# Kernel optimization log

Measured on AMD Instinct MI355X. Metric: run time of the kernel, lower is better.

Reference implementation:

```python
import jax, jax.numpy as jnp
import numpy as np

B, T, N, F, E, L = 2, 2, 10000, 128, 160000, 2


def setup_inputs() -> dict:
    key = jax.random.key(0)
    k = jax.random.split(key, 6)
    feature = jax.random.normal(k[0], (B, T, N, F), jnp.float32)
    edge_src = jax.random.randint(k[1], (E,), 0, N, jnp.int32)
    edge_dst = jax.random.randint(k[2], (E,), 0, N, jnp.int32)
    s = 1.0 / np.sqrt(F).astype(np.float32)
    W_self = jax.random.normal(k[3], (L, F, F), jnp.float32) * s
    W_neigh = jax.random.normal(k[4], (L, F, F), jnp.float32) * s
    b = jnp.zeros((L, F), jnp.float32)
    return dict(feature=feature, W_self=W_self, W_neigh=W_neigh, b=b,
                edge_src=edge_src, edge_dst=edge_dst)


def reference(feature, W_self, W_neigh, b, edge_src, edge_dst):
    # feature: [B, T, N, Fin]; edge (src -> dst) as in dgl.from_scipy(csr).
    Bs, Ts, Ns, Fin = feature.shape
    num_layers = W_self.shape[0]
    # in-degree per dst node; mean over zero in-degree nodes is 0 (DGL semantics)
    deg = jax.ops.segment_sum(jnp.ones(edge_dst.shape, jnp.float32), edge_dst,
                              num_segments=Ns)
    inv_deg = jnp.where(deg > 0, 1.0 / jnp.maximum(deg, 1.0), 0.0)  # [N]
    # node-major layout for gather/scatter: [N, B, T, F]
    h = jnp.transpose(feature, (2, 0, 1, 3))
    for l in range(num_layers):
        msg = h[edge_src]  # [E, B, T, F] irregular gather
        agg = jax.ops.segment_sum(msg, edge_dst, num_segments=Ns)
        h_neigh = agg * inv_deg[:, None, None, None]  # mean aggregation
        h = (jnp.einsum('nbtf,fg->nbtg', h, W_self[l])
             + jnp.einsum('nbtf,fg->nbtg', h_neigh, W_neigh[l])
             + b[l])
    # res.permute(0,2,1,3) in torch -> [B, T, N, Fout]
    return jnp.transpose(h, (1, 2, 0, 3))
```

## Files before the change

kernel.cpp:

```cpp
#include <hip/hip_runtime.h>

constexpr int N_  = 10000;
constexpr int F_  = 128;
constexpr int E_  = 160000;
constexpr int BT_ = 4;
constexpr int M_  = N_ * BT_;
constexpr int CAP = 64;

typedef __attribute__((ext_vector_type(8))) short bf16x8;
typedef __attribute__((ext_vector_type(4))) float f32x4;
typedef __attribute__((ext_vector_type(2))) float f32x2;
typedef __attribute__((ext_vector_type(8))) unsigned short u16x8;

static __device__ inline unsigned short f2bf(float f) {
    union { float f; unsigned int i; } v; v.f = f;
    unsigned int x = v.i;
    return (unsigned short)((x + 0x7fffu + ((x >> 16) & 1u)) >> 16);
}


__global__ __launch_bounds__(256) void k_pre(const float4* __restrict__ feat,
        unsigned short* __restrict__ h0, unsigned char* __restrict__ h8,
        unsigned char* __restrict__ h18z,
        const int* __restrict__ src, const int* __restrict__ dst,
        int* __restrict__ cursor, int* __restrict__ bucket,
        const float* __restrict__ Wself, const float* __restrict__ Wneigh,
        unsigned short* __restrict__ Wp) {
    const int b = blockIdx.x;
    const int tid = threadIdx.x;
    if (b < 625) {
        int e = b * 256 + tid;
        int d = dst[e];
        int p = atomicAdd(&cursor[d], 1);
        if (p < CAP) bucket[d * CAP + p] = src[e];
    } else if (b < 657) {
        if (b == 625) {
            if (tid < 64) {
                uint2 z; z.x = 0u; z.y = 0u;
                *(uint2*)(h8 + (size_t)N_ * 512 + tid * 8) = z;
            } else if (tid < 128) {
                uint2 z; z.x = 0u; z.y = 0u;
                *(uint2*)(h18z + (size_t)N_ * 512 + (tid - 64) * 8) = z;
            }
        }
        int t = (b - 625) * 256 + tid;
        int mat = t >> 11;
        int r = t & 2047;
        int kb = r >> 9;
        int nb = (r >> 6) & 7;
        int lane = r & 63;
        int l = mat >> 1, s = mat & 1;
        const float* W = (s ? Wneigh : Wself) + (size_t)l * F_ * F_;
        int k0 = kb * 32 + (lane >> 4) * 8;
        int n  = nb * 16 + (lane & 15);
        unsigned short* dstp = Wp + (size_t)mat * 16384 +
                               (size_t)((kb * 8 + nb) * 64 + lane) * 8;
#pragma unroll
        for (int j = 0; j < 8; j++) dstp[j] = f2bf(W[(size_t)(k0 + j) * F_ + n]);
    } else {
        int i = (b - 657) * 256 + tid;
        int f4 = i & 31;
        int m  = i >> 5;
        int n  = m >> 2;
        int bt = m & 3;
        float4 v = feat[(bt * N_ + n) * 32 + f4];
        ushort4 o;
        o.x = f2bf(v.x); o.y = f2bf(v.y); o.z = f2bf(v.z); o.w = f2bf(v.w);
        *(ushort4*)(h0 + (size_t)m * 128 + f4 * 4) = o;
        int w0 = __builtin_amdgcn_cvt_pk_fp8_f32(v.x, v.y, 0, false);
        int w1 = __builtin_amdgcn_cvt_pk_fp8_f32(v.z, v.w, w0, true);
        *(unsigned int*)(h8 + (size_t)m * 128 + f4 * 4) = (unsigned int)w1;
    }
}


template <bool LAST>
__global__ __launch_bounds__(256) void k_fused(const unsigned short* __restrict__ h,
        const unsigned char* __restrict__ g8, unsigned char* __restrict__ s8out,
        const int* __restrict__ cursor, const int* __restrict__ bucket,
        const unsigned short* __restrict__ Wp, const float* __restrict__ bias,
        void* __restrict__ outv) {
    __shared__ unsigned short aggs[4][4][136];
    const int tid  = threadIdx.x;
    const int wave = tid >> 6, lane = tid & 63;
    const int m0   = blockIdx.x * 16;
    const int node0 = m0 >> 2;
    const int col  = lane & 15;
    const int quad = lane >> 4;

    const unsigned short* A0 = h + (size_t)(m0 + col) * 128 + quad * 8;
    bf16x8 aA[4];
#pragma unroll
    for (int kb = 0; kb < 4; kb++) aA[kb] = *(const bf16x8*)(A0 + kb * 32);

    const int n   = node0 + wave;
    const int deg = cursor[n];
    const int nn  = deg < CAP ? deg : CAP;
    const int nn8 = (nn + 7) & ~7;
    int idx = bucket[n * CAP + (lane < nn ? lane : 0)];

    float acc8[8] = {0.f, 0.f, 0.f, 0.f, 0.f, 0.f, 0.f, 0.f};
    for (int e0 = 0; e0 < nn8; e0 += 8) {
#pragma unroll
        for (int u = 0; u < 8; u++) {
            int e = e0 + u;
            int s = (e < nn) ? __builtin_amdgcn_readlane(idx, e) : N_;
            uint2 a8 = *(const uint2*)(g8 + (size_t)s * 512 + lane * 8);
            f32x2 p0 = __builtin_amdgcn_cvt_pk_f32_fp8(a8.x, false);
            f32x2 p1 = __builtin_amdgcn_cvt_pk_f32_fp8(a8.x, true);
            f32x2 p2 = __builtin_amdgcn_cvt_pk_f32_fp8(a8.y, false);
            f32x2 p3 = __builtin_amdgcn_cvt_pk_f32_fp8(a8.y, true);
            acc8[0] += p0.x; acc8[1] += p0.y;
            acc8[2] += p1.x; acc8[3] += p1.y;
            acc8[4] += p2.x; acc8[5] += p2.y;
            acc8[6] += p3.x; acc8[7] += p3.y;
        }
    }
    {
        float w = (deg > 0) ? 1.0f / (float)deg : 0.0f;
        u16x8 o;
#pragma unroll
        for (int j = 0; j < 8; j++) o[j] = f2bf(acc8[j] * w);
        *(u16x8*)&aggs[wave][lane >> 4][(lane & 15) * 8] = o;
    }
    __syncthreads();

    const int np = wave;
    f32x4 acc[2];
#pragma unroll
    for (int j = 0; j < 2; j++) {
        float b = bias[(np * 2 + j) * 16 + col];
        acc[j] = (f32x4){b, b, b, b};
    }

    const unsigned short* As = &aggs[col >> 2][col & 3][quad * 8];
    const unsigned short* B0 = Wp + (size_t)lane * 8;
    const unsigned short* B1 = B0 + 16384;

#pragma unroll
    for (int kb = 0; kb < 4; kb++) {
        bf16x8 a = aA[kb];
#pragma unroll
        for (int j = 0; j < 2; j++) {
            int nb = np * 2 + j;
            bf16x8 b = *(const bf16x8*)(B0 + (size_t)((kb * 8 + nb) * 64) * 8);
            acc[j] = __builtin_amdgcn_mfma_f32_16x16x32_bf16(a, b, acc[j], 0, 0, 0);
        }
    }
#pragma unroll
    for (int kb = 0; kb < 4; kb++) {
        bf16x8 a = *(const bf16x8*)(As + kb * 32);
#pragma unroll
        for (int j = 0; j < 2; j++) {
            int nb = np * 2 + j;
            bf16x8 b = *(const bf16x8*)(B1 + (size_t)((kb * 8 + nb) * 64) * 8);
            acc[j] = __builtin_amdgcn_mfma_f32_16x16x32_bf16(a, b, acc[j], 0, 0, 0);
        }
    }

    if (LAST) {
        float* out = (float*)outv;
#pragma unroll
        for (int j = 0; j < 2; j++) {
            int nb = np * 2 + j;
#pragma unroll
            for (int r = 0; r < 4; r++) {
                int m = m0 + quad * 4 + r;
                int node = m >> 2, bt = m & 3;
                out[((size_t)bt * N_ + node) * 128 + nb * 16 + col] = acc[j][r];
            }
        }
    } else {
        unsigned short* out = (unsigned short*)outv;
#pragma unroll
        for (int j = 0; j < 2; j++) {
            int nb = np * 2 + j;
#pragma unroll
            for (int r = 0; r < 4; r++) {
                int m = m0 + quad * 4 + r;
                out[(size_t)m * 128 + nb * 16 + col] = f2bf(acc[j][r]);
                int p = __builtin_amdgcn_cvt_pk_fp8_f32(acc[j][r], acc[j][r],
                                                        0, false);
                s8out[(size_t)m * 128 + nb * 16 + col] = (unsigned char)(p & 0xff);
            }
        }
    }
}


extern "C" void kernel_launch(void* const* d_in, const int* in_sizes, int n_in,
                              void* d_out, int out_size, void* d_ws, size_t ws_size,
                              hipStream_t stream) {
    const float* feature = (const float*)d_in[0];
    const float* W_self  = (const float*)d_in[1];
    const float* W_neigh = (const float*)d_in[2];
    const float* bias    = (const float*)d_in[3];
    const int*   e_src   = (const int*)d_in[4];
    const int*   e_dst   = (const int*)d_in[5];
    float*       out     = (float*)d_out;

    char* ws = (char*)d_ws;
    unsigned short* h0   = (unsigned short*)ws;  ws += (size_t)M_ * F_ * 2;
    unsigned short* h1   = (unsigned short*)ws;  ws += (size_t)M_ * F_ * 2;
    unsigned char*  h08  = (unsigned char*)ws;   ws += (size_t)M_ * F_ + 512;
    unsigned char*  h18  = (unsigned char*)ws;   ws += (size_t)M_ * F_ + 512;
    unsigned short* Wp   = (unsigned short*)ws;  ws += (size_t)4 * 16384 * 2;
    int*   cursor  = (int*)ws;                   ws += (size_t)N_ * 4;
    int*   bucket  = (int*)ws;                   ws += (size_t)N_ * CAP * 4;

    hipMemsetAsync(cursor, 0, (size_t)N_ * 4, stream);

    k_pre<<<5657, 256, 0, stream>>>((const float4*)feature, h0, h08, h18, e_src,
                                    e_dst, cursor, bucket, W_self, W_neigh, Wp);

    const int gb = M_ / 16;
    k_fused<false><<<gb, 256, 0, stream>>>(h0, h08, h18, cursor, bucket, Wp,
                                           bias, h1);
    k_fused<true><<<gb, 256, 0, stream>>>(h1, h18, nullptr, cursor, bucket,
                                          Wp + 2 * 16384, bias + F_, out);
}
```

Baseline: 139.8 us.

## Drop bf16 h0 copy and read fp32 features directly in first layer

The preprocessing kernel no longer writes a bf16 copy of the input features. It only emits the fp8 gather copy, with each thread now converting 8 values instead of 4. The first fused layer reads the fp32 feature tensor directly in its original [B,T,N,F] layout and converts it to bf16 in registers, which removes one full write and read of the intermediate. The neighbor gather loop is also unrolled by 4 instead of 8, which cuts wasted padded iterations but leaves fewer loads in flight.

```diff
diff --git a/kernel.cpp b/kernel.cpp
--- a/kernel.cpp
+++ b/kernel.cpp
@@ -12,6 +12,8 @@
 typedef __attribute__((ext_vector_type(2))) float f32x2;
 typedef __attribute__((ext_vector_type(8))) unsigned short u16x8;
 
+union bfu { u16x8 u; bf16x8 s; };
+
 static __device__ inline unsigned short f2bf(float f) {
     union { float f; unsigned int i; } v; v.f = f;
     unsigned int x = v.i;
@@ -20,8 +22,7 @@
 
 
 __global__ __launch_bounds__(256) void k_pre(const float4* __restrict__ feat,
-        unsigned short* __restrict__ h0, unsigned char* __restrict__ h8,
-        unsigned char* __restrict__ h18z,
+        unsigned char* __restrict__ h8, unsigned char* __restrict__ h18z,
         const int* __restrict__ src, const int* __restrict__ dst,
         int* __restrict__ cursor, int* __restrict__ bucket,
         const float* __restrict__ Wself, const float* __restrict__ Wneigh,
@@ -59,23 +60,25 @@
         for (int j = 0; j < 8; j++) dstp[j] = f2bf(W[(size_t)(k0 + j) * F_ + n]);
     } else {
         int i = (b - 657) * 256 + tid;
-        int f4 = i & 31;
-        int m  = i >> 5;
+        int c8 = i & 15;
+        int m  = i >> 4;
         int n  = m >> 2;
         int bt = m & 3;
-        float4 v = feat[(bt * N_ + n) * 32 + f4];
-        ushort4 o;
-        o.x = f2bf(v.x); o.y = f2bf(v.y); o.z = f2bf(v.z); o.w = f2bf(v.w);
-        *(ushort4*)(h0 + (size_t)m * 128 + f4 * 4) = o;
-        int w0 = __builtin_amdgcn_cvt_pk_fp8_f32(v.x, v.y, 0, false);
-        int w1 = __builtin_amdgcn_cvt_pk_fp8_f32(v.z, v.w, w0, true);
-        *(unsigned int*)(h8 + (size_t)m * 128 + f4 * 4) = (unsigned int)w1;
-    }
-}
-
-
-template <bool LAST>
-__global__ __launch_bounds__(256) void k_fused(const unsigned short* __restrict__ h,
+        const float4* p = feat + ((size_t)(bt * N_ + n) * 32 + c8 * 2);
+        float4 v0 = p[0];
+        float4 v1 = p[1];
+        int w0 = __builtin_amdgcn_cvt_pk_fp8_f32(v0.x, v0.y, 0, false);
+        int w1 = __builtin_amdgcn_cvt_pk_fp8_f32(v0.z, v0.w, w0, true);
+        int w2 = __builtin_amdgcn_cvt_pk_fp8_f32(v1.x, v1.y, 0, false);
+        int w3 = __builtin_amdgcn_cvt_pk_fp8_f32(v1.z, v1.w, w2, true);
+        uint2 o; o.x = (unsigned int)w1; o.y = (unsigned int)w3;
+        *(uint2*)(h8 + (size_t)m * 128 + c8 * 8) = o;
+    }
+}
+
+
+template <bool FP32A, bool LAST>
+__global__ __launch_bounds__(256) void k_fused(const void* __restrict__ hA,
         const unsigned char* __restrict__ g8, unsigned char* __restrict__ s8out,
         const int* __restrict__ cursor, const int* __restrict__ bucket,
         const unsigned short* __restrict__ Wp, const float* __restrict__ bias,
@@ -88,21 +91,40 @@
     const int col  = lane & 15;
     const int quad = lane >> 4;
 
-    const unsigned short* A0 = h + (size_t)(m0 + col) * 128 + quad * 8;
     bf16x8 aA[4];
-#pragma unroll
-    for (int kb = 0; kb < 4; kb++) aA[kb] = *(const bf16x8*)(A0 + kb * 32);
+    if (FP32A) {
+        const int m = m0 + col;
+        const int an = m >> 2, abt = m & 3;
+        const float* Af = (const float*)hA +
+                          ((size_t)(abt * N_ + an) * 128 + quad * 8);
+#pragma unroll
+        for (int kb = 0; kb < 4; kb++) {
+            float4 u0 = *(const float4*)(Af + kb * 32);
+            float4 u1 = *(const float4*)(Af + kb * 32 + 4);
+            bfu t;
+            t.u[0] = f2bf(u0.x); t.u[1] = f2bf(u0.y);
+            t.u[2] = f2bf(u0.z); t.u[3] = f2bf(u0.w);
+            t.u[4] = f2bf(u1.x); t.u[5] = f2bf(u1.y);
+            t.u[6] = f2bf(u1.z); t.u[7] = f2bf(u1.w);
+            aA[kb] = t.s;
+        }
+    } else {
+        const unsigned short* A0 = (const unsigned short*)hA +
+                                   (size_t)(m0 + col) * 128 + quad * 8;
+#pragma unroll
+        for (int kb = 0; kb < 4; kb++) aA[kb] = *(const bf16x8*)(A0 + kb * 32);
+    }
 
     const int n   = node0 + wave;
     const int deg = cursor[n];
     const int nn  = deg < CAP ? deg : CAP;
-    const int nn8 = (nn + 7) & ~7;
+    const int nn4 = (nn + 3) & ~3;
     int idx = bucket[n * CAP + (lane < nn ? lane : 0)];
 
     float acc8[8] = {0.f, 0.f, 0.f, 0.f, 0.f, 0.f, 0.f, 0.f};
-    for (int e0 = 0; e0 < nn8; e0 += 8) {
-#pragma unroll
-        for (int u = 0; u < 8; u++) {
+    for (int e0 = 0; e0 < nn4; e0 += 4) {
+#pragma unroll
+        for (int u = 0; u < 4; u++) {
             int e = e0 + u;
             int s = (e < nn) ? __builtin_amdgcn_readlane(idx, e) : N_;
             uint2 a8 = *(const uint2*)(g8 + (size_t)s * 512 + lane * 8);
@@ -200,7 +222,6 @@
     float*       out     = (float*)d_out;
 
     char* ws = (char*)d_ws;
-    unsigned short* h0   = (unsigned short*)ws;  ws += (size_t)M_ * F_ * 2;
     unsigned short* h1   = (unsigned short*)ws;  ws += (size_t)M_ * F_ * 2;
     unsigned char*  h08  = (unsigned char*)ws;   ws += (size_t)M_ * F_ + 512;
     unsigned char*  h18  = (unsigned char*)ws;   ws += (size_t)M_ * F_ + 512;
@@ -210,12 +231,13 @@
 
     hipMemsetAsync(cursor, 0, (size_t)N_ * 4, stream);
 
-    k_pre<<<5657, 256, 0, stream>>>((const float4*)feature, h0, h08, h18, e_src,
+    k_pre<<<3157, 256, 0, stream>>>((const float4*)feature, h08, h18, e_src,
                                     e_dst, cursor, bucket, W_self, W_neigh, Wp);
 
     const int gb = M_ / 16;
-    k_fused<false><<<gb, 256, 0, stream>>>(h0, h08, h18, cursor, bucket, Wp,
-                                           bias, h1);
-    k_fused<true><<<gb, 256, 0, stream>>>(h1, h18, nullptr, cursor, bucket,
-                                          Wp + 2 * 16384, bias + F_, out);
-}
+    k_fused<true, false><<<gb, 256, 0, stream>>>(feature, h08, h18, cursor,
+                                                 bucket, Wp, bias, h1);
+    k_fused<false, true><<<gb, 256, 0, stream>>>(h1, h18, nullptr, cursor,
+                                                 bucket, Wp + 2 * 16384,
+                                                 bias + F_, out);
+}
```

New measurement: 139.3 us. Within noise of the previous version (-0.3%).
